# Performance work log

Hardware: AMD Instinct MI355X
Metric: run time of the kernel (lower is better)

## Reference

```python
import jax, jax.numpy as jnp
import numpy as np
import math

H = 1024
B = 16
DEPTH = 5
BEAM = 3
EPS = 1e-5  # nn.LayerNorm default eps
UCB_C = 1.414


def setup_inputs() -> dict:
    key = jax.random.key(0)
    ks = jax.random.split(key, 8)
    return {
        "problem_embedding": jax.random.normal(ks[0], (B, H), jnp.float32),
        "context": jax.random.normal(ks[1], (B, H), jnp.float32),
        # thought_encoder: Linear(2H -> H) + GELU + LayerNorm(H)
        "W_te": jax.random.normal(ks[2], (2 * H, H), jnp.float32) / math.sqrt(2 * H),
        "b_te": jnp.zeros((H,), jnp.float32),
        "g_ln": jnp.ones((H,), jnp.float32),
        "b_ln": jnp.zeros((H,), jnp.float32),
        # value_head: Linear(H -> 1)
        "w_v": jax.random.normal(ks[3], (H,), jnp.float32) / math.sqrt(H),
        "b_v": jnp.zeros((), jnp.float32),
        # expansion_net: beam_width x [Linear(H->2H), GELU, Linear(2H->H)], stacked
        "W1": jax.random.normal(ks[4], (BEAM, 2 * H, H), jnp.float32) / math.sqrt(H),
        "b1": jnp.zeros((BEAM, 2 * H), jnp.float32),
        "W2": jax.random.normal(ks[5], (BEAM, H, 2 * H), jnp.float32) / math.sqrt(2 * H),
        "b2": jnp.zeros((BEAM, H), jnp.float32),
        "num_simulations": 25,
    }


def _gelu(x):
    return jax.nn.gelu(x, approximate=False)  # torch nn.GELU default = exact erf


def _layernorm(x, g, b):
    mu = jnp.mean(x, -1, keepdims=True)
    var = jnp.mean((x - mu) ** 2, -1, keepdims=True)
    return g * (x - mu) * jax.lax.rsqrt(var + EPS) + b


def _forward(problem_embedding, context, W_te, b_te, g_ln, b_ln, w_v, b_v, W1, b1, W2, b2, num_simulations):
    MAX = 1 + num_simulations * DEPTH * BEAM  # upper bound on tree size
    BP = int(math.ceil(math.log(MAX) / math.log(BEAM))) + 2  # parent-chain length bound
    neg_inf = jnp.float32(-jnp.inf)

    def value(e):
        return e @ w_v + b_v

    def search(p, c):
        root = _layernorm(_gelu(jnp.concatenate([p, c]) @ W_te + b_te), g_ln, b_ln)
        emb = jnp.zeros((MAX, H), jnp.float32).at[0].set(root)
        vals = jnp.zeros((MAX,), jnp.float32).at[0].set(value(root))
        visits = jnp.zeros((MAX,), jnp.int32).at[0].set(1)
        n = jnp.int32(1)

        def sim(carry, _):
            emb, vals, visits, n = carry
            cur = jnp.int32(0)
            for d in range(DEPTH):
                cur_emb = emb[cur]
                # expansion condition exactly as in torch (len(tree)-1 < (idx+1)*beam)
                expand = (n - 1) < (cur + 1) * BEAM
                h = _gelu(jnp.einsum('whd,d->wh', W1, cur_emb) + b1)      # [BEAM, 2H]
                new_emb = cur_emb + 0.1 * (jnp.einsum('wdh,wh->wd', W2, h) + b2)  # [BEAM, H]
                new_vals = new_emb @ w_v + b_v                             # [BEAM]
                idx = jnp.where(expand, n + jnp.arange(BEAM, dtype=jnp.int32), MAX)
                emb = emb.at[idx].set(new_emb, mode='drop')
                vals = vals.at[idx].set(new_vals, mode='drop')
                visits = visits.at[idx].set(1, mode='drop')
                n = n + jnp.where(expand, BEAM, 0).astype(jnp.int32)
                if d < DEPTH - 1:
                    # parent_visits = sum(visits[cur*beam : (cur+1)*beam]) (python slice clamps to len)
                    pidx = cur * BEAM + jnp.arange(BEAM, dtype=jnp.int32)
                    pv = jnp.sum(jnp.where(pidx < n, visits[jnp.minimum(pidx, MAX - 1)], 0))
                    log_pv = jnp.log(jnp.maximum(pv, 1).astype(jnp.float32))
                    best_idx, best = cur, neg_inf
                    for ci in range(BEAM):
                        child = cur * BEAM + 1 + ci
                        safe = jnp.minimum(child, MAX - 1)
                        cn = jnp.maximum(visits[safe], 1).astype(jnp.float32)  # visits >= 1 always
                        ucb = vals[safe] + UCB_C * jnp.sqrt(log_pv / cn)
                        ucb = jnp.where(child < n, ucb, neg_inf)
                        better = ucb > best
                        best = jnp.where(better, ucb, best)
                        best_idx = jnp.where(better, child, best_idx)
                    cur = best_idx
            leaf = jnp.minimum(cur, n - 1)
            leaf_val = vals[leaf]

            def bp(_, st):
                node, vals_, visits_ = st
                parent = (node - 1) // BEAM
                active = node > 0
                pc = visits_[parent].astype(jnp.float32)
                upd = (vals_[parent] * pc + leaf_val) / (pc + 1.0)
                vals_ = jnp.where(active, vals_.at[parent].set(upd), vals_)
                visits_ = jnp.where(active, visits_.at[parent].add(1), visits_)
                node = jnp.where(active, parent, node)
                return node, vals_, visits_

            _, vals, visits = jax.lax.fori_loop(0, BP, bp, (leaf, vals, visits))
            visits = visits.at[leaf].add(1)
            return (emb, vals, visits, n), None

        (emb, vals, visits, n), _ = jax.lax.scan(sim, (emb, vals, visits, n), None, length=num_simulations)
        mvals = jnp.where(jnp.arange(MAX) < n, vals, neg_inf)
        best = jnp.argmax(mvals)  # first max, matching strict-> loop
        return emb[best], mvals[best]

    final_emb, best_vals = jax.vmap(search)(problem_embedding, context)
    confidence = jnp.minimum(best_vals / (jnp.max(best_vals) + 1e-8), 1.0)[:, None]
    return final_emb, confidence, best_vals


def reference(problem_embedding, context, W_te, b_te, g_ln, b_ln, w_v, b_v, W1, b1, W2, b2, num_simulations):
    return _forward(problem_embedding, context, W_te, b_te, g_ln, b_ln, w_v, b_v,
                    W1, b1, W2, b2, int(num_simulations))
```

## Files before the change

kernel.cpp:

```cpp
#include <hip/hip_runtime.h>
#include <hip/hip_fp16.h>

#define Hh 1024
#define H2 2048
#define NB 16
#define MAXN 376
#define NSTAGE 125

__device__ __forceinline__ float gelu_f(float x) {
    return 0.5f * x * (1.0f + erff(x * 0.70710678118654752440f));
}

__global__ __launch_bounds__(256) void kcvt(const float* __restrict__ src,
                                            __half* __restrict__ dst, int n) {
    int i = blockIdx.x * 256 + threadIdx.x;
    int stride = gridDim.x * 256;
    for (; i < n; i += stride) dst[i] = __float2half(src[i]);
}

__global__ __launch_bounds__(256) void k0a(const float* __restrict__ Wte,
                                           const float* __restrict__ bte,
                                           const float* __restrict__ pe,
                                           const float* __restrict__ cte,
                                           float* __restrict__ tmp) {
    __shared__ float red[8][8][33];
    int tid = threadIdx.x;
    int ob = blockIdx.x & 31, bg = blockIdx.x >> 5;
    int o_l = tid & 31, kc = tid >> 5;
    int o = ob * 32 + o_l;
    float acc[8] = {0.f,0.f,0.f,0.f,0.f,0.f,0.f,0.f};
    const float* src = (kc < 4) ? pe : cte;
    int koff = (kc < 4) ? 0 : 1024;
    int k0 = kc * 256;
    for (int k = k0; k < k0 + 256; k += 4) {
        float w0 = Wte[(size_t)(k + 0) * Hh + o];
        float w1 = Wte[(size_t)(k + 1) * Hh + o];
        float w2 = Wte[(size_t)(k + 2) * Hh + o];
        float w3 = Wte[(size_t)(k + 3) * Hh + o];
#pragma unroll
        for (int bb = 0; bb < 8; ++bb) {
            int b = bg * 8 + bb;
            const float4 x4 = *(const float4*)(src + (size_t)b * Hh + (k - koff));
            acc[bb] = fmaf(w3, x4.w, fmaf(w2, x4.z, fmaf(w1, x4.y, fmaf(w0, x4.x, acc[bb]))));
        }
    }
#pragma unroll
    for (int bb = 0; bb < 8; ++bb) red[kc][bb][o_l] = acc[bb];
    __syncthreads();
    int o2 = tid & 31, bb2 = tid >> 5;
    float s = 0.f;
#pragma unroll
    for (int q = 0; q < 8; ++q) s += red[q][bb2][o2];
    int og = ob * 32 + o2;
    int b = bg * 8 + bb2;
    tmp[(size_t)b * Hh + og] = gelu_f(s + bte[og]);
}

__global__ __launch_bounds__(256) void k0b(const float* __restrict__ tmp,
                                           const float* __restrict__ g,
                                           const float* __restrict__ bl,
                                           const float* __restrict__ wv,
                                           const float* __restrict__ bv,
                                           float* __restrict__ emb,
                                           float* __restrict__ vals,
                                           int* __restrict__ visits,
                                           int* __restrict__ nbuf,
                                           int* __restrict__ curbuf,
                                           float* __restrict__ vacc) {
    __shared__ float red[256];
    int b = blockIdx.x, tid = threadIdx.x;
    for (int q = tid; q < MAXN; q += 256) {
        if (q > 0) { vals[b * MAXN + q] = 0.f; visits[b * MAXN + q] = 0; }
    }
    if (b == 0 && tid < 96) vacc[tid] = 0.f;
    float4 v = *(const float4*)(tmp + (size_t)b * Hh + tid * 4);
    red[tid] = (v.x + v.y) + (v.z + v.w);
    __syncthreads();
    for (int st = 128; st > 0; st >>= 1) { if (tid < st) red[tid] += red[tid + st]; __syncthreads(); }
    float mu = red[0] * (1.0f / 1024.0f);
    __syncthreads();
    float dx0 = v.x - mu, dx1 = v.y - mu, dx2 = v.z - mu, dx3 = v.w - mu;
    red[tid] = (dx0 * dx0 + dx1 * dx1) + (dx2 * dx2 + dx3 * dx3);
    __syncthreads();
    for (int st = 128; st > 0; st >>= 1) { if (tid < st) red[tid] += red[tid + st]; __syncthreads(); }
    float var = red[0] * (1.0f / 1024.0f);
    __syncthreads();
    float rs = rsqrtf(var + 1e-5f);
    int d0 = tid * 4;
    float r0 = g[d0 + 0] * (dx0 * rs) + bl[d0 + 0];
    float r1 = g[d0 + 1] * (dx1 * rs) + bl[d0 + 1];
    float r2 = g[d0 + 2] * (dx2 * rs) + bl[d0 + 2];
    float r3 = g[d0 + 3] * (dx3 * rs) + bl[d0 + 3];
    float4 ro; ro.x = r0; ro.y = r1; ro.z = r2; ro.w = r3;
    *(float4*)(emb + (size_t)b * MAXN * Hh + d0) = ro;
    red[tid] = (r0 * wv[d0] + r1 * wv[d0 + 1]) + (r2 * wv[d0 + 2] + r3 * wv[d0 + 3]);
    __syncthreads();
    for (int st = 128; st > 0; st >>= 1) { if (tid < st) red[tid] += red[tid + st]; __syncthreads(); }
    if (tid == 0) {
        vals[b * MAXN] = red[0] + bv[0];
        visits[b * MAXN] = 1;
        nbuf[b] = 1;
        curbuf[b] = 0;
    }
}

__global__ __launch_bounds__(256) void k_mv1(const __half* __restrict__ W1h,
                                             const float* __restrict__ b1,
                                             const float* __restrict__ emb,
                                             float* __restrict__ hbuf,
                                             const float* __restrict__ vacc_in,
                                             float* __restrict__ vacc_out,
                                             float* vals, int* visits,
                                             const int* __restrict__ nin,
                                             const int* __restrict__ curin,
                                             int* __restrict__ nout,
                                             int* __restrict__ curout,
                                             const float* __restrict__ bv, int t) {
    __shared__ float red[64][4][17];
    __shared__ int curL[NB];
    __shared__ int exS;
    int tid = threadIdx.x;
    int d = t % 5;
    if (blockIdx.x == 0 && tid < 48) vacc_out[tid] = 0.f;
    int row = tid >> 6, kpos = tid & 63;
    int o = blockIdx.x * 4 + row;
    const __half* wp = W1h + (size_t)o * Hh;
    uint4 wl0 = *(const uint4*)(wp + kpos * 8);
    uint4 wl1 = *(const uint4*)(wp + 512 + kpos * 8);
    if (tid == 0) exS = 0;
    __syncthreads();
    if (tid < NB) {
        int b = tid;
        int n_old = nin[b], cur_old = curin[b];
        int n_new = n_old;
        bool ep = false;
        float vnew0 = 0.f, vnew1 = 0.f, vnew2 = 0.f;
        if (t > 0) {
            ep = (n_old - 1) < (cur_old + 1) * 3;
            if (ep) {
                vnew0 = bv[0] + vacc_in[b * 3 + 0];
                vnew1 = bv[0] + vacc_in[b * 3 + 1];
                vnew2 = bv[0] + vacc_in[b * 3 + 2];
                n_new += 3;
            }
        }
        int cur_new = 0;
        const float* vb = vals + b * MAXN;
        const int* tb = visits + b * MAXN;
        if (d != 0) {
            int pv = 0;
#pragma unroll
            for (int i = 0; i < 3; ++i) {
                int pidx = 3 * cur_old + i;
                if (pidx < n_new) {
                    int safe = min(pidx, MAXN - 1);
                    int jj = safe - n_old;
                    int vis = (ep && jj >= 0 && jj < 3) ? 1 : tb[safe];
                    pv += vis;
                }
            }
            float log_pv = logf((float)(pv > 1 ? pv : 1));
            float best = -INFINITY; int best_idx = cur_old;
#pragma unroll
            for (int ci = 0; ci < 3; ++ci) {
                int child = 3 * cur_old + 1 + ci;
                int safe = min(child, MAXN - 1);
                int jj = safe - n_old;
                float v; int cn;
                if (ep && jj >= 0 && jj < 3) {
                    v = (jj == 0) ? vnew0 : ((jj == 1) ? vnew1 : vnew2);
                    cn = 1;
                } else { v = vb[safe]; cn = tb[safe]; }
                float cnf = (float)(cn > 1 ? cn : 1);
                float ucb = v + 1.414f * sqrtf(log_pv / cnf);
                if (child < n_new && ucb > best) { best = ucb; best_idx = child; }
            }
            cur_new = best_idx;
        } else if (t > 0 && blockIdx.x == 0) {
            float* vbw = vals + b * MAXN;
            int* tbw = visits + b * MAXN;
            int leaf = min(cur_old, n_new - 1);
            float lv = vbw[leaf];
            int node = leaf;
#pragma unroll
            for (int it = 0; it < 8; ++it) {
                if (node > 0) {
                    int p = (node - 1) / 3;
                    int pc = tbw[p];
                    float pcf = (float)pc;
                    vbw[p] = (vbw[p] * pcf + lv) / (pcf + 1.0f);
                    tbw[p] = pc + 1;
                    node = p;
                }
            }
            tbw[leaf] += 1;
        }
        bool ex = (n_new - 1) < (cur_new + 1) * 3;
        curL[b] = cur_new;
        if (ex) atomicOr(&exS, 1 << b);
        if (blockIdx.x == 0) {
            nout[b] = n_new; curout[b] = cur_new;
            if (ep) {
                if (n_old + 0 < MAXN) { vals[b * MAXN + n_old + 0] = vnew0; visits[b * MAXN + n_old + 0] = 1; }
                if (n_old + 1 < MAXN) { vals[b * MAXN + n_old + 1] = vnew1; visits[b * MAXN + n_old + 1] = 1; }
                if (n_old + 2 < MAXN) { vals[b * MAXN + n_old + 2] = vnew2; visits[b * MAXN + n_old + 2] = 1; }
            }
        }
    }
    __syncthreads();
    unsigned em = (unsigned)exS;
    float acc[16];
#pragma unroll
    for (int b = 0; b < 16; ++b) acc[b] = 0.f;
    if (em) {
        const float4* xp[16];
#pragma unroll
        for (int b = 0; b < 16; ++b)
            xp[b] = (const float4*)(emb + (size_t)(b * MAXN + curL[b]) * Hh);
        union { uint4 u; __half h[8]; } wu[2];
        wu[0].u = wl0; wu[1].u = wl1;
#pragma unroll
        for (int j = 0; j < 2; ++j) {
            float wf[8];
#pragma unroll
            for (int r = 0; r < 8; ++r) wf[r] = __half2float(wu[j].h[r]);
            int f4 = j * 128 + kpos * 2;
#pragma unroll
            for (int b = 0; b < 16; ++b) {
                if (em & (1u << b)) {
                    float4 xa = xp[b][f4];
                    float4 xb = xp[b][f4 + 1];
                    acc[b] = fmaf(wf[3], xa.w, fmaf(wf[2], xa.z, fmaf(wf[1], xa.y, fmaf(wf[0], xa.x, acc[b]))));
                    acc[b] = fmaf(wf[7], xb.w, fmaf(wf[6], xb.z, fmaf(wf[5], xb.y, fmaf(wf[4], xb.x, acc[b]))));
                }
            }
        }
    }
    {
        float* rp = red[kpos][row];
#pragma unroll
        for (int b = 0; b < 16; ++b) rp[b] = acc[b];
    }
    __syncthreads();
    if (tid < 64) {
        int row2 = tid >> 4, b2 = tid & 15;
        if (em & (1u << b2)) {
            float s = 0.f;
#pragma unroll
            for (int q = 0; q < 64; ++q) s += red[q][row2][b2];
            int og = blockIdx.x * 4 + row2;
            int w = og >> 11, ii = og & 2047;
            float hv = gelu_f(s + b1[og]);
            hbuf[(size_t)(b2 * 3 + w) * H2 + ii] = hv;
        }
    }
}

__global__ __launch_bounds__(256) void k_mv2(const __half* __restrict__ W2h,
                                             const float* __restrict__ b2p,
                                             const float* __restrict__ wv,
                                             const float* __restrict__ hbuf,
                                             float* __restrict__ emb,
                                             float* __restrict__ vacc,
                                             const int* __restrict__ nin,
                                             const int* __restrict__ curin) {
    __shared__ float red[128][2][17];
    __shared__ float prS[16][3];
    __shared__ int curL[NB], nL[NB];
    __shared__ int exS;
    int tid = threadIdx.x;
    int row = tid >> 7, kpos = tid & 127;
    int o = blockIdx.x * 2 + row;
    const __half* wp = W2h + (size_t)o * H2;
    uint4 wl0 = *(const uint4*)(wp + kpos * 8);
    uint4 wl1 = *(const uint4*)(wp + 1024 + kpos * 8);
    if (tid < NB) { curL[tid] = curin[tid]; nL[tid] = nin[tid]; }
    __syncthreads();
    if (tid == 0) {
        int m = 0;
        for (int b = 0; b < NB; ++b)
            if ((nL[b] - 1) < (curL[b] + 1) * 3) m |= 1 << b;
        exS = m;
    }
    __syncthreads();
    unsigned em = (unsigned)exS;
    int w = o >> 10;
    float acc[16];
#pragma unroll
    for (int b = 0; b < 16; ++b) acc[b] = 0.f;
    if (em) {
        const float4* hp[16];
#pragma unroll
        for (int b = 0; b < 16; ++b) hp[b] = (const float4*)(hbuf + (size_t)(b * 3 + w) * H2);
        union { uint4 u; __half h[8]; } wu[2];
        wu[0].u = wl0; wu[1].u = wl1;
#pragma unroll
        for (int j = 0; j < 2; ++j) {
            float wf[8];
#pragma unroll
            for (int r = 0; r < 8; ++r) wf[r] = __half2float(wu[j].h[r]);
            int f4 = j * 256 + kpos * 2;
#pragma unroll
            for (int b = 0; b < 16; ++b) {
                if (em & (1u << b)) {
                    float4 ha = hp[b][f4];
                    float4 hb = hp[b][f4 + 1];
                    acc[b] = fmaf(wf[3], ha.w, fmaf(wf[2], ha.z, fmaf(wf[1], ha.y, fmaf(wf[0], ha.x, acc[b]))));
                    acc[b] = fmaf(wf[7], hb.w, fmaf(wf[6], hb.z, fmaf(wf[5], hb.y, fmaf(wf[4], hb.x, acc[b]))));
                }
            }
        }
    }
    {
        float* rp = red[kpos][row];
#pragma unroll
        for (int b = 0; b < 16; ++b) rp[b] = acc[b];
    }
    __syncthreads();
    if (tid < 32) {
        int row2 = tid >> 4, b2 = tid & 15;
        int og = blockIdx.x * 2 + row2;
        int w2i = og >> 10, d2 = og & 1023;
        float pr = 0.f;
        if (em & (1u << b2)) {
            float s = 0.f;
#pragma unroll
            for (int q = 0; q < 128; ++q) s += red[q][row2][b2];
            float ce = emb[(size_t)(b2 * MAXN + curL[b2]) * Hh + d2];
            float nv = ce + 0.1f * (s + b2p[og]);
            int nidx = nL[b2] + w2i;
            if (nidx < MAXN) emb[(size_t)(b2 * MAXN + nidx) * Hh + d2] = nv;
            pr = nv * wv[d2];
        }
        prS[b2][row2] = pr;
    }
    __syncthreads();
    if (tid < NB) {
        if (em & (1u << tid)) {
            float s = prS[tid][0] + prS[tid][1];
            int wblk = (blockIdx.x * 2) >> 10;
            atomicAdd(&vacc[tid * 3 + wblk], s);
        }
    }
}

__global__ __launch_bounds__(256) void kf(const float* __restrict__ emb,
                                          float* vals, int* visits,
                                          const int* __restrict__ nin,
                                          const int* __restrict__ curin,
                                          const float* __restrict__ vacc,
                                          const float* __restrict__ bv,
                                          float* __restrict__ out) {
    __shared__ int nF[NB];
    __shared__ float bval[NB];
    __shared__ int bidx[NB];
    __shared__ float redv[NB][16];
    __shared__ int redi[NB][16];
    __shared__ float mxS;
    int tid = threadIdx.x;
    if (tid < NB) {
        int b = tid;
        int n_old = nin[b], cur_old = curin[b];
        int n_new = n_old;
        bool ep = (n_old - 1) < (cur_old + 1) * 3;
        if (ep) {
            float vn0 = bv[0] + vacc[b * 3 + 0];
            float vn1 = bv[0] + vacc[b * 3 + 1];
            float vn2 = bv[0] + vacc[b * 3 + 2];
            if (n_old + 0 < MAXN) { vals[b * MAXN + n_old + 0] = vn0; visits[b * MAXN + n_old + 0] = 1; }
            if (n_old + 1 < MAXN) { vals[b * MAXN + n_old + 1] = vn1; visits[b * MAXN + n_old + 1] = 1; }
            if (n_old + 2 < MAXN) { vals[b * MAXN + n_old + 2] = vn2; visits[b * MAXN + n_old + 2] = 1; }
            n_new += 3;
        }
        int leaf = min(cur_old, n_new - 1);
        float lv = vals[b * MAXN + leaf];
        int node = leaf;
#pragma unroll
        for (int it = 0; it < 8; ++it) {
            if (node > 0) {
                int p = (node - 1) / 3;
                int pc = visits[b * MAXN + p];
                float pcf = (float)pc;
                vals[b * MAXN + p] = (vals[b * MAXN + p] * pcf + lv) / (pcf + 1.0f);
                visits[b * MAXN + p] = pc + 1;
                node = p;
            }
        }
        visits[b * MAXN + leaf] += 1;
        nF[b] = n_new;
    }
    __syncthreads();
    {
        int b = tid >> 4, q = tid & 15;
        float bv_ = -INFINITY; int bi_ = MAXN;
        int nn = nF[b];
        for (int idx = q; idx < MAXN; idx += 16) {
            float v = (idx < nn) ? vals[b * MAXN + idx] : -INFINITY;
            if (v > bv_ || (v == bv_ && idx < bi_)) { bv_ = v; bi_ = idx; }
        }
        redv[b][q] = bv_; redi[b][q] = bi_;
    }
    __syncthreads();
    if (tid < NB) {
        int b = tid;
        float bb = -INFINITY; int bi = MAXN;
        for (int q = 0; q < 16; ++q) {
            float v = redv[b][q]; int i2 = redi[b][q];
            if (v > bb || (v == bb && i2 < bi)) { bb = v; bi = i2; }
        }
        bval[b] = bb; bidx[b] = bi;
    }
    __syncthreads();
    if (tid == 0) {
        float m = bval[0];
        for (int b = 1; b < NB; ++b) m = fmaxf(m, bval[b]);
        mxS = m;
    }
    __syncthreads();
    if (tid < NB) {
        float c = bval[tid] / (mxS + 1e-8f);
        out[16384 + tid] = fminf(c, 1.0f);
        out[16400 + tid] = bval[tid];
    }
    for (int q2 = tid; q2 < 16384; q2 += 256) {
        int b = q2 >> 10, dd = q2 & 1023;
        out[q2] = emb[(size_t)(b * MAXN + bidx[b]) * Hh + dd];
    }
}

extern "C" void kernel_launch(void* const* d_in, const int* in_sizes, int n_in,
                              void* d_out, int out_size, void* d_ws, size_t ws_size,
                              hipStream_t stream) {
    const float* pe  = (const float*)d_in[0];
    const float* ce  = (const float*)d_in[1];
    const float* Wte = (const float*)d_in[2];
    const float* bte = (const float*)d_in[3];
    const float* gln = (const float*)d_in[4];
    const float* bln = (const float*)d_in[5];
    const float* wv  = (const float*)d_in[6];
    const float* bv  = (const float*)d_in[7];
    const float* W1  = (const float*)d_in[8];
    const float* b1  = (const float*)d_in[9];
    const float* W2  = (const float*)d_in[10];
    const float* b2  = (const float*)d_in[11];
    float* out = (float*)d_out;

    float* ws = (float*)d_ws;
    __half* W1h = (__half*)ws;
    __half* W2h = W1h + 6291456;
    float* embb = ws + 6291456;
    float* hbuf = embb + 6160384;
    float* vacc = hbuf + 98304;
    float* tmp  = vacc + 96;
    float* vals = tmp + 16384;
    int* visits = (int*)(vals + 6016);
    int* nbuf   = visits + 6016;
    int* curbuf = nbuf + 32;

    hipLaunchKernelGGL(kcvt, dim3(2048), dim3(256), 0, stream, W1, W1h, 6291456);
    hipLaunchKernelGGL(kcvt, dim3(2048), dim3(256), 0, stream, W2, W2h, 6291456);

    hipLaunchKernelGGL(k0a, dim3(64), dim3(256), 0, stream, Wte, bte, pe, ce, tmp);
    hipLaunchKernelGGL(k0b, dim3(16), dim3(256), 0, stream, tmp, gln, bln, wv, bv,
                       embb, vals, visits, nbuf, curbuf, vacc);

    for (int t = 0; t < NSTAGE; ++t) {
        int si = t & 1, so = si ^ 1;
        bool dead = (t > 0) && (t % 5 == 0);
        hipLaunchKernelGGL(k_mv1, dim3(dead ? 1 : 1536), dim3(256), 0, stream,
                           W1h, b1, embb, hbuf,
                           vacc + ((t ^ 1) & 1) * 48,
                           vacc + (t & 1) * 48,
                           vals, visits,
                           nbuf + si * 16, curbuf + si * 16,
                           nbuf + so * 16, curbuf + so * 16, bv, t);
        if (!dead)
            hipLaunchKernelGGL(k_mv2, dim3(1536), dim3(256), 0, stream,
                               W2h, b2, wv, hbuf, embb,
                               vacc + (t & 1) * 48,
                               nbuf + so * 16, curbuf + so * 16);
    }
    hipLaunchKernelGGL(kf, dim3(1), dim3(256), 0, stream,
                       embb, vals, visits, nbuf + 16, curbuf + 16, vacc, bv, out);
}
```

Baseline: 3.409 ms.

## Fold dead backprop stage into adjacent matvec kernels and prewarm fp16 weights

Removes the single-block dead launch at each simulation boundary. Its backpropagation is now recomputed locally in k_mv1, with root-level stats held in registers, and committed to global memory by block 0 of the following k_mv2. This needs triple-buffered n/cur state. A warm-up kernel also reads both fp16 weight copies to prime the cache before the loop. The cost is added control-flow complexity and a redundant read pass over the weights.

```diff
diff --git a/kernel.cpp b/kernel.cpp
--- a/kernel.cpp
+++ b/kernel.cpp
@@ -16,6 +16,16 @@
     int i = blockIdx.x * 256 + threadIdx.x;
     int stride = gridDim.x * 256;
     for (; i < n; i += stride) dst[i] = __float2half(src[i]);
+}
+
+__global__ __launch_bounds__(256) void kwarm(const uint4* __restrict__ a,
+                                             const uint4* __restrict__ b,
+                                             int n16, float* __restrict__ sink) {
+    int i = blockIdx.x * 256 + threadIdx.x;
+    int s = gridDim.x * 256;
+    unsigned acc = 0;
+    for (int j = i; j < n16; j += s) { uint4 x = a[j]; uint4 y = b[j]; acc ^= x.x ^ y.x; }
+    if (acc == 0xdeadbeefu) sink[0] = 1.f;
 }
 
 __global__ __launch_bounds__(256) void k0a(const float* __restrict__ Wte,
@@ -108,20 +118,20 @@
                                              const float* __restrict__ b1,
                                              const float* __restrict__ emb,
                                              float* __restrict__ hbuf,
-                                             const float* __restrict__ vacc_in,
-                                             float* __restrict__ vacc_out,
+                                             const float* __restrict__ vin,
+                                             float* __restrict__ vout,
                                              float* vals, int* visits,
                                              const int* __restrict__ nin,
                                              const int* __restrict__ curin,
                                              int* __restrict__ nout,
                                              int* __restrict__ curout,
-                                             const float* __restrict__ bv, int t) {
+                                             const float* __restrict__ bv, int t, int fold) {
     __shared__ float red[64][4][17];
     __shared__ int curL[NB];
     __shared__ int exS;
     int tid = threadIdx.x;
     int d = t % 5;
-    if (blockIdx.x == 0 && tid < 48) vacc_out[tid] = 0.f;
+    if (blockIdx.x == 0 && tid < 48) vout[tid] = 0.f;
     int row = tid >> 6, kpos = tid & 63;
     int o = blockIdx.x * 4 + row;
     const __half* wp = W1h + (size_t)o * Hh;
@@ -132,15 +142,45 @@
     if (tid < NB) {
         int b = tid;
         int n_old = nin[b], cur_old = curin[b];
+        float val03[4]; int vis03[4];
+        bool lcl = false;
+        if (fold) {
+            bool epA = (n_old - 1) < (cur_old + 1) * 3;
+            float a0 = 0.f, a1 = 0.f, a2 = 0.f;
+            if (epA) { a0 = bv[0] + vin[b*3+0]; a1 = bv[0] + vin[b*3+1]; a2 = bv[0] + vin[b*3+2]; }
+            int nA = n_old + (epA ? 3 : 0);
+#pragma unroll
+            for (int i = 0; i < 4; ++i) { val03[i] = vals[b*MAXN+i]; vis03[i] = visits[b*MAXN+i]; }
+            int leaf = min(cur_old, nA - 1);
+            int jl = leaf - n_old;
+            float lv;
+            if (epA && jl >= 0 && jl < 3) lv = (jl == 0) ? a0 : ((jl == 1) ? a1 : a2);
+            else lv = vals[b*MAXN + min(leaf, MAXN-1)];
+            int node = leaf;
+#pragma unroll
+            for (int it2 = 0; it2 < 8; ++it2) {
+                if (node > 0) {
+                    int p = (node - 1) / 3;
+                    int pc; float pvv;
+                    if (p < 4) { pc = vis03[p]; pvv = val03[p]; }
+                    else { pc = visits[b*MAXN+p]; pvv = vals[b*MAXN+p]; }
+                    float pcf = (float)pc;
+                    float nvv = (pvv * pcf + lv) / (pcf + 1.0f);
+                    if (p < 4) { val03[p] = nvv; vis03[p] = pc + 1; }
+                    node = p;
+                }
+            }
+            n_old = nA; cur_old = 0; lcl = true;
+        }
         int n_new = n_old;
         bool ep = false;
         float vnew0 = 0.f, vnew1 = 0.f, vnew2 = 0.f;
-        if (t > 0) {
+        if (t > 0 && !fold) {
             ep = (n_old - 1) < (cur_old + 1) * 3;
             if (ep) {
-                vnew0 = bv[0] + vacc_in[b * 3 + 0];
-                vnew1 = bv[0] + vacc_in[b * 3 + 1];
-                vnew2 = bv[0] + vacc_in[b * 3 + 2];
+                vnew0 = bv[0] + vin[b*3+0];
+                vnew1 = bv[0] + vin[b*3+1];
+                vnew2 = bv[0] + vin[b*3+2];
                 n_new += 3;
             }
         }
@@ -155,7 +195,10 @@
                 if (pidx < n_new) {
                     int safe = min(pidx, MAXN - 1);
                     int jj = safe - n_old;
-                    int vis = (ep && jj >= 0 && jj < 3) ? 1 : tb[safe];
+                    int vis;
+                    if (ep && jj >= 0 && jj < 3) vis = 1;
+                    else if (lcl && safe < 4) vis = vis03[safe];
+                    else vis = tb[safe];
                     pv += vis;
                 }
             }
@@ -170,30 +213,14 @@
                 if (ep && jj >= 0 && jj < 3) {
                     v = (jj == 0) ? vnew0 : ((jj == 1) ? vnew1 : vnew2);
                     cn = 1;
+                } else if (lcl && safe < 4) {
+                    v = val03[safe]; cn = vis03[safe];
                 } else { v = vb[safe]; cn = tb[safe]; }
                 float cnf = (float)(cn > 1 ? cn : 1);
                 float ucb = v + 1.414f * sqrtf(log_pv / cnf);
                 if (child < n_new && ucb > best) { best = ucb; best_idx = child; }
             }
             cur_new = best_idx;
-        } else if (t > 0 && blockIdx.x == 0) {
-            float* vbw = vals + b * MAXN;
-            int* tbw = visits + b * MAXN;
-            int leaf = min(cur_old, n_new - 1);
-            float lv = vbw[leaf];
-            int node = leaf;
-#pragma unroll
-            for (int it = 0; it < 8; ++it) {
-                if (node > 0) {
-                    int p = (node - 1) / 3;
-                    int pc = tbw[p];
-                    float pcf = (float)pc;
-                    vbw[p] = (vbw[p] * pcf + lv) / (pcf + 1.0f);
-                    tbw[p] = pc + 1;
-                    node = p;
-                }
-            }
-            tbw[leaf] += 1;
         }
         bool ex = (n_new - 1) < (cur_new + 1) * 3;
         curL[b] = cur_new;
@@ -263,12 +290,47 @@
                                              float* __restrict__ emb,
                                              float* __restrict__ vacc,
                                              const int* __restrict__ nin,
-                                             const int* __restrict__ curin) {
+                                             const int* __restrict__ curin,
+                                             int foldA,
+                                             const int* __restrict__ ninA,
+                                             const int* __restrict__ curinA,
+                                             const float* __restrict__ vinA,
+                                             float* vals, int* visits,
+                                             const float* __restrict__ bv) {
     __shared__ float red[128][2][17];
     __shared__ float prS[16][3];
     __shared__ int curL[NB], nL[NB];
     __shared__ int exS;
     int tid = threadIdx.x;
+    if (foldA && blockIdx.x == 0 && tid < NB) {
+        int b = tid;
+        int nO = ninA[b], cO = curinA[b];
+        bool epA = (nO - 1) < (cO + 1) * 3;
+        if (epA) {
+            float a0 = bv[0] + vinA[b*3+0];
+            float a1 = bv[0] + vinA[b*3+1];
+            float a2 = bv[0] + vinA[b*3+2];
+            if (nO + 0 < MAXN) { vals[b*MAXN+nO+0] = a0; visits[b*MAXN+nO+0] = 1; }
+            if (nO + 1 < MAXN) { vals[b*MAXN+nO+1] = a1; visits[b*MAXN+nO+1] = 1; }
+            if (nO + 2 < MAXN) { vals[b*MAXN+nO+2] = a2; visits[b*MAXN+nO+2] = 1; }
+        }
+        int nA = nO + (epA ? 3 : 0);
+        int leaf = min(cO, nA - 1);
+        float lv = vals[b*MAXN + min(leaf, MAXN-1)];
+        int node = leaf;
+#pragma unroll
+        for (int it2 = 0; it2 < 8; ++it2) {
+            if (node > 0) {
+                int p = (node - 1) / 3;
+                int pc = visits[b*MAXN+p];
+                float pcf = (float)pc;
+                vals[b*MAXN+p] = (vals[b*MAXN+p] * pcf + lv) / (pcf + 1.0f);
+                visits[b*MAXN+p] = pc + 1;
+                node = p;
+            }
+        }
+        visits[b*MAXN+leaf] += 1;
+    }
     int row = tid >> 7, kpos = tid & 127;
     int o = blockIdx.x * 2 + row;
     const __half* wp = W2h + (size_t)o * H2;
@@ -455,31 +517,40 @@
     float* vals = tmp + 16384;
     int* visits = (int*)(vals + 6016);
     int* nbuf   = visits + 6016;
-    int* curbuf = nbuf + 32;
+    int* curbuf = nbuf + 48;
+    float* sink = (float*)(curbuf + 48);
 
     hipLaunchKernelGGL(kcvt, dim3(2048), dim3(256), 0, stream, W1, W1h, 6291456);
     hipLaunchKernelGGL(kcvt, dim3(2048), dim3(256), 0, stream, W2, W2h, 6291456);
+    hipLaunchKernelGGL(kwarm, dim3(2048), dim3(256), 0, stream,
+                       (const uint4*)W1h, (const uint4*)W2h, 786432, sink);
 
     hipLaunchKernelGGL(k0a, dim3(64), dim3(256), 0, stream, Wte, bte, pe, ce, tmp);
     hipLaunchKernelGGL(k0b, dim3(16), dim3(256), 0, stream, tmp, gln, bln, wv, bv,
                        embb, vals, visits, nbuf, curbuf, vacc);
 
+    int L = 0;
     for (int t = 0; t < NSTAGE; ++t) {
-        int si = t & 1, so = si ^ 1;
-        bool dead = (t > 0) && (t % 5 == 0);
-        hipLaunchKernelGGL(k_mv1, dim3(dead ? 1 : 1536), dim3(256), 0, stream,
+        if (t > 0 && t % 5 == 0) continue;
+        int fold = (t % 5 == 1 && t > 1) ? 1 : 0;
+        int rs = (fold ? (t - 1) : t) % 3;
+        int wsS = (t + 1) % 3;
+        int vi = ((L + 1) & 1) * 48;
+        int vo = (L & 1) * 48;
+        hipLaunchKernelGGL(k_mv1, dim3(1536), dim3(256), 0, stream,
                            W1h, b1, embb, hbuf,
-                           vacc + ((t ^ 1) & 1) * 48,
-                           vacc + (t & 1) * 48,
+                           vacc + vi, vacc + vo,
                            vals, visits,
-                           nbuf + si * 16, curbuf + si * 16,
-                           nbuf + so * 16, curbuf + so * 16, bv, t);
-        if (!dead)
-            hipLaunchKernelGGL(k_mv2, dim3(1536), dim3(256), 0, stream,
-                               W2h, b2, wv, hbuf, embb,
-                               vacc + (t & 1) * 48,
-                               nbuf + so * 16, curbuf + so * 16);
+                           nbuf + rs * 16, curbuf + rs * 16,
+                           nbuf + wsS * 16, curbuf + wsS * 16, bv, t, fold);
+        hipLaunchKernelGGL(k_mv2, dim3(1536), dim3(256), 0, stream,
+                           W2h, b2, wv, hbuf, embb,
+                           vacc + vo,
+                           nbuf + wsS * 16, curbuf + wsS * 16,
+                           fold, nbuf + rs * 16, curbuf + rs * 16, vacc + vi,
+                           vals, visits, bv);
+        ++L;
     }
     hipLaunchKernelGGL(kf, dim3(1), dim3(256), 0, stream,
-                       embb, vals, visits, nbuf + 16, curbuf + 16, vacc, bv, out);
-}
+                       embb, vals, visits, nbuf + 32, curbuf + 32, vacc, bv, out);
+}
```

New measurement: 3.412 ms. Within noise of the previous version (+0.1%).

## Split tree bookkeeping into single-block kernel and double matvec rows per block

Applied to the files above, without the earlier changes.

Moves the per-stage MCTS selection, expansion and backprop bookkeeping out of the first matvec kernel into a tiny one-block kernel. That kernel publishes a control buffer (expansion mask, current node and node count), which both matvec kernels read instead of recomputing it. The dead depth-0 stage launches are folded into the next stage's bookkeeping. Each matvec block now handles twice as many output rows with 4 weight vectors per thread, so half as many blocks are launched. This adds one small serial launch per stage in exchange for removing redundant per-block bookkeeping and skipped launches, and it lowers parallelism per launch.

```diff
diff --git a/kernel.cpp b/kernel.cpp
--- a/kernel.cpp
+++ b/kernel.cpp
@@ -72,7 +72,7 @@
     for (int q = tid; q < MAXN; q += 256) {
         if (q > 0) { vals[b * MAXN + q] = 0.f; visits[b * MAXN + q] = 0; }
     }
-    if (b == 0 && tid < 96) vacc[tid] = 0.f;
+    if (b == 0 && tid < 48) vacc[tid] = 0.f;
     float4 v = *(const float4*)(tmp + (size_t)b * Hh + tid * 4);
     red[tid] = (v.x + v.y) + (v.z + v.w);
     __syncthreads();
@@ -104,127 +104,117 @@
     }
 }
 
+__global__ __launch_bounds__(64) void kbook(float* vals, int* visits,
+                                            int* nbuf, int* curbuf,
+                                            float* vacc, int* ctrl,
+                                            const float* __restrict__ bv,
+                                            int t, int fold) {
+    __shared__ int exArr[NB];
+    int tid = threadIdx.x;
+    if (tid < NB) {
+        int b = tid;
+        int n = nbuf[b], cur = curbuf[b];
+        float* vb = vals + b * MAXN;
+        int* tb = visits + b * MAXN;
+        float v0 = vacc[b * 3 + 0], v1 = vacc[b * 3 + 1], v2 = vacc[b * 3 + 2];
+        if (fold) {
+            bool epA = (n - 1) < (cur + 1) * 3;
+            if (epA) {
+                if (n + 0 < MAXN) { vb[n + 0] = bv[0] + v0; tb[n + 0] = 1; }
+                if (n + 1 < MAXN) { vb[n + 1] = bv[0] + v1; tb[n + 1] = 1; }
+                if (n + 2 < MAXN) { vb[n + 2] = bv[0] + v2; tb[n + 2] = 1; }
+                n += 3;
+            }
+            int leaf = min(cur, n - 1);
+            float lv = vb[min(leaf, MAXN - 1)];
+            int node = leaf;
+#pragma unroll
+            for (int it = 0; it < 8; ++it) {
+                if (node > 0) {
+                    int p = (node - 1) / 3;
+                    int pc = tb[p];
+                    float pcf = (float)pc;
+                    vb[p] = (vb[p] * pcf + lv) / (pcf + 1.0f);
+                    tb[p] = pc + 1;
+                    node = p;
+                }
+            }
+            tb[leaf] += 1;
+            cur = 0;
+        } else if (t > 0) {
+            bool ep = (n - 1) < (cur + 1) * 3;
+            if (ep) {
+                if (n + 0 < MAXN) { vb[n + 0] = bv[0] + v0; tb[n + 0] = 1; }
+                if (n + 1 < MAXN) { vb[n + 1] = bv[0] + v1; tb[n + 1] = 1; }
+                if (n + 2 < MAXN) { vb[n + 2] = bv[0] + v2; tb[n + 2] = 1; }
+                n += 3;
+            }
+        }
+        int d = t % 5;
+        int cur_new = 0;
+        if (d != 0) {
+            int pv = 0;
+#pragma unroll
+            for (int i = 0; i < 3; ++i) {
+                int pidx = 3 * cur + i;
+                if (pidx < n) pv += tb[min(pidx, MAXN - 1)];
+            }
+            float log_pv = logf((float)(pv > 1 ? pv : 1));
+            float best = -INFINITY; int best_idx = cur;
+#pragma unroll
+            for (int ci = 0; ci < 3; ++ci) {
+                int child = 3 * cur + 1 + ci;
+                int safe = min(child, MAXN - 1);
+                float v = vb[safe]; int cn = tb[safe];
+                float cnf = (float)(cn > 1 ? cn : 1);
+                float ucb = v + 1.414f * sqrtf(log_pv / cnf);
+                if (child < n && ucb > best) { best = ucb; best_idx = child; }
+            }
+            cur_new = best_idx;
+        }
+        nbuf[b] = n; curbuf[b] = cur_new;
+        ctrl[1 + b] = cur_new;
+        ctrl[17 + b] = n;
+        exArr[b] = ((n - 1) < (cur_new + 1) * 3) ? 1 : 0;
+    }
+    __syncthreads();
+    if (tid == 0) {
+        int m = 0;
+        for (int b = 0; b < NB; ++b) if (exArr[b]) m |= (1 << b);
+        ctrl[0] = m;
+    }
+    if (tid < 48) vacc[tid] = 0.f;
+}
+
 __global__ __launch_bounds__(256) void k_mv1(const __half* __restrict__ W1h,
                                              const float* __restrict__ b1,
                                              const float* __restrict__ emb,
                                              float* __restrict__ hbuf,
-                                             const float* __restrict__ vacc_in,
-                                             float* __restrict__ vacc_out,
-                                             float* vals, int* visits,
-                                             const int* __restrict__ nin,
-                                             const int* __restrict__ curin,
-                                             int* __restrict__ nout,
-                                             int* __restrict__ curout,
-                                             const float* __restrict__ bv, int t) {
-    __shared__ float red[64][4][17];
-    __shared__ int curL[NB];
-    __shared__ int exS;
+                                             const int* __restrict__ ctrl) {
+    __shared__ float red[32][8][17];
     int tid = threadIdx.x;
-    int d = t % 5;
-    if (blockIdx.x == 0 && tid < 48) vacc_out[tid] = 0.f;
-    int row = tid >> 6, kpos = tid & 63;
-    int o = blockIdx.x * 4 + row;
+    int row = tid >> 5, kpos = tid & 31;
+    int o = blockIdx.x * 8 + row;
     const __half* wp = W1h + (size_t)o * Hh;
-    uint4 wl0 = *(const uint4*)(wp + kpos * 8);
-    uint4 wl1 = *(const uint4*)(wp + 512 + kpos * 8);
-    if (tid == 0) exS = 0;
-    __syncthreads();
-    if (tid < NB) {
-        int b = tid;
-        int n_old = nin[b], cur_old = curin[b];
-        int n_new = n_old;
-        bool ep = false;
-        float vnew0 = 0.f, vnew1 = 0.f, vnew2 = 0.f;
-        if (t > 0) {
-            ep = (n_old - 1) < (cur_old + 1) * 3;
-            if (ep) {
-                vnew0 = bv[0] + vacc_in[b * 3 + 0];
-                vnew1 = bv[0] + vacc_in[b * 3 + 1];
-                vnew2 = bv[0] + vacc_in[b * 3 + 2];
-                n_new += 3;
-            }
-        }
-        int cur_new = 0;
-        const float* vb = vals + b * MAXN;
-        const int* tb = visits + b * MAXN;
-        if (d != 0) {
-            int pv = 0;
-#pragma unroll
-            for (int i = 0; i < 3; ++i) {
-                int pidx = 3 * cur_old + i;
-                if (pidx < n_new) {
-                    int safe = min(pidx, MAXN - 1);
-                    int jj = safe - n_old;
-                    int vis = (ep && jj >= 0 && jj < 3) ? 1 : tb[safe];
-                    pv += vis;
-                }
-            }
-            float log_pv = logf((float)(pv > 1 ? pv : 1));
-            float best = -INFINITY; int best_idx = cur_old;
-#pragma unroll
-            for (int ci = 0; ci < 3; ++ci) {
-                int child = 3 * cur_old + 1 + ci;
-                int safe = min(child, MAXN - 1);
-                int jj = safe - n_old;
-                float v; int cn;
-                if (ep && jj >= 0 && jj < 3) {
-                    v = (jj == 0) ? vnew0 : ((jj == 1) ? vnew1 : vnew2);
-                    cn = 1;
-                } else { v = vb[safe]; cn = tb[safe]; }
-                float cnf = (float)(cn > 1 ? cn : 1);
-                float ucb = v + 1.414f * sqrtf(log_pv / cnf);
-                if (child < n_new && ucb > best) { best = ucb; best_idx = child; }
-            }
-            cur_new = best_idx;
-        } else if (t > 0 && blockIdx.x == 0) {
-            float* vbw = vals + b * MAXN;
-            int* tbw = visits + b * MAXN;
-            int leaf = min(cur_old, n_new - 1);
-            float lv = vbw[leaf];
-            int node = leaf;
-#pragma unroll
-            for (int it = 0; it < 8; ++it) {
-                if (node > 0) {
-                    int p = (node - 1) / 3;
-                    int pc = tbw[p];
-                    float pcf = (float)pc;
-                    vbw[p] = (vbw[p] * pcf + lv) / (pcf + 1.0f);
-                    tbw[p] = pc + 1;
-                    node = p;
-                }
-            }
-            tbw[leaf] += 1;
-        }
-        bool ex = (n_new - 1) < (cur_new + 1) * 3;
-        curL[b] = cur_new;
-        if (ex) atomicOr(&exS, 1 << b);
-        if (blockIdx.x == 0) {
-            nout[b] = n_new; curout[b] = cur_new;
-            if (ep) {
-                if (n_old + 0 < MAXN) { vals[b * MAXN + n_old + 0] = vnew0; visits[b * MAXN + n_old + 0] = 1; }
-                if (n_old + 1 < MAXN) { vals[b * MAXN + n_old + 1] = vnew1; visits[b * MAXN + n_old + 1] = 1; }
-                if (n_old + 2 < MAXN) { vals[b * MAXN + n_old + 2] = vnew2; visits[b * MAXN + n_old + 2] = 1; }
-            }
-        }
-    }
-    __syncthreads();
-    unsigned em = (unsigned)exS;
-    float acc[16];
-#pragma unroll
-    for (int b = 0; b < 16; ++b) acc[b] = 0.f;
+    uint4 wl[4];
+#pragma unroll
+    for (int j = 0; j < 4; ++j) wl[j] = *(const uint4*)(wp + j * 256 + kpos * 8);
+    unsigned em = (unsigned)ctrl[0];
     if (em) {
         const float4* xp[16];
 #pragma unroll
         for (int b = 0; b < 16; ++b)
-            xp[b] = (const float4*)(emb + (size_t)(b * MAXN + curL[b]) * Hh);
-        union { uint4 u; __half h[8]; } wu[2];
-        wu[0].u = wl0; wu[1].u = wl1;
-#pragma unroll
-        for (int j = 0; j < 2; ++j) {
+            xp[b] = (const float4*)(emb + (size_t)(b * MAXN + ctrl[1 + b]) * Hh);
+        float acc[16];
+#pragma unroll
+        for (int b = 0; b < 16; ++b) acc[b] = 0.f;
+#pragma unroll
+        for (int j = 0; j < 4; ++j) {
+            union { uint4 u; __half h[8]; } wu; wu.u = wl[j];
             float wf[8];
 #pragma unroll
-            for (int r = 0; r < 8; ++r) wf[r] = __half2float(wu[j].h[r]);
-            int f4 = j * 128 + kpos * 2;
+            for (int r = 0; r < 8; ++r) wf[r] = __half2float(wu.h[r]);
+            int f4 = j * 64 + kpos * 2;
 #pragma unroll
             for (int b = 0; b < 16; ++b) {
                 if (em & (1u << b)) {
@@ -235,20 +225,18 @@
                 }
             }
         }
-    }
-    {
         float* rp = red[kpos][row];
 #pragma unroll
         for (int b = 0; b < 16; ++b) rp[b] = acc[b];
     }
     __syncthreads();
-    if (tid < 64) {
+    if (em && tid < 128) {
         int row2 = tid >> 4, b2 = tid & 15;
         if (em & (1u << b2)) {
             float s = 0.f;
 #pragma unroll
-            for (int q = 0; q < 64; ++q) s += red[q][row2][b2];
-            int og = blockIdx.x * 4 + row2;
+            for (int q = 0; q < 32; ++q) s += red[q][row2][b2];
+            int og = blockIdx.x * 8 + row2;
             int w = og >> 11, ii = og & 2047;
             float hv = gelu_f(s + b1[og]);
             hbuf[(size_t)(b2 * 3 + w) * H2 + ii] = hv;
@@ -262,44 +250,33 @@
                                              const float* __restrict__ hbuf,
                                              float* __restrict__ emb,
                                              float* __restrict__ vacc,
-                                             const int* __restrict__ nin,
-                                             const int* __restrict__ curin) {
-    __shared__ float red[128][2][17];
-    __shared__ float prS[16][3];
-    __shared__ int curL[NB], nL[NB];
-    __shared__ int exS;
+                                             const int* __restrict__ ctrl) {
+    __shared__ float red[64][4][17];
+    __shared__ float prS[16][5];
     int tid = threadIdx.x;
-    int row = tid >> 7, kpos = tid & 127;
-    int o = blockIdx.x * 2 + row;
+    int row = tid >> 6, kpos = tid & 63;
+    int o = blockIdx.x * 4 + row;
     const __half* wp = W2h + (size_t)o * H2;
-    uint4 wl0 = *(const uint4*)(wp + kpos * 8);
-    uint4 wl1 = *(const uint4*)(wp + 1024 + kpos * 8);
-    if (tid < NB) { curL[tid] = curin[tid]; nL[tid] = nin[tid]; }
-    __syncthreads();
-    if (tid == 0) {
-        int m = 0;
-        for (int b = 0; b < NB; ++b)
-            if ((nL[b] - 1) < (curL[b] + 1) * 3) m |= 1 << b;
-        exS = m;
-    }
-    __syncthreads();
-    unsigned em = (unsigned)exS;
+    uint4 wl[4];
+#pragma unroll
+    for (int j = 0; j < 4; ++j) wl[j] = *(const uint4*)(wp + j * 512 + kpos * 8);
+    unsigned em = (unsigned)ctrl[0];
     int w = o >> 10;
-    float acc[16];
-#pragma unroll
-    for (int b = 0; b < 16; ++b) acc[b] = 0.f;
     if (em) {
         const float4* hp[16];
 #pragma unroll
-        for (int b = 0; b < 16; ++b) hp[b] = (const float4*)(hbuf + (size_t)(b * 3 + w) * H2);
-        union { uint4 u; __half h[8]; } wu[2];
-        wu[0].u = wl0; wu[1].u = wl1;
-#pragma unroll
-        for (int j = 0; j < 2; ++j) {
+        for (int b = 0; b < 16; ++b)
+            hp[b] = (const float4*)(hbuf + (size_t)(b * 3 + w) * H2);
+        float acc[16];
+#pragma unroll
+        for (int b = 0; b < 16; ++b) acc[b] = 0.f;
+#pragma unroll
+        for (int j = 0; j < 4; ++j) {
+            union { uint4 u; __half h[8]; } wu; wu.u = wl[j];
             float wf[8];
 #pragma unroll
-            for (int r = 0; r < 8; ++r) wf[r] = __half2float(wu[j].h[r]);
-            int f4 = j * 256 + kpos * 2;
+            for (int r = 0; r < 8; ++r) wf[r] = __half2float(wu.h[r]);
+            int f4 = j * 128 + kpos * 2;
 #pragma unroll
             for (int b = 0; b < 16; ++b) {
                 if (em & (1u << b)) {
@@ -310,37 +287,32 @@
                 }
             }
         }
-    }
-    {
         float* rp = red[kpos][row];
 #pragma unroll
         for (int b = 0; b < 16; ++b) rp[b] = acc[b];
     }
     __syncthreads();
-    if (tid < 32) {
+    if (em && tid < 64) {
         int row2 = tid >> 4, b2 = tid & 15;
-        int og = blockIdx.x * 2 + row2;
+        int og = blockIdx.x * 4 + row2;
         int w2i = og >> 10, d2 = og & 1023;
         float pr = 0.f;
         if (em & (1u << b2)) {
             float s = 0.f;
 #pragma unroll
-            for (int q = 0; q < 128; ++q) s += red[q][row2][b2];
-            float ce = emb[(size_t)(b2 * MAXN + curL[b2]) * Hh + d2];
+            for (int q = 0; q < 64; ++q) s += red[q][row2][b2];
+            float ce = emb[(size_t)(b2 * MAXN + ctrl[1 + b2]) * Hh + d2];
             float nv = ce + 0.1f * (s + b2p[og]);
-            int nidx = nL[b2] + w2i;
+            int nidx = ctrl[17 + b2] + w2i;
             if (nidx < MAXN) emb[(size_t)(b2 * MAXN + nidx) * Hh + d2] = nv;
             pr = nv * wv[d2];
         }
         prS[b2][row2] = pr;
     }
     __syncthreads();
-    if (tid < NB) {
-        if (em & (1u << tid)) {
-            float s = prS[tid][0] + prS[tid][1];
-            int wblk = (blockIdx.x * 2) >> 10;
-            atomicAdd(&vacc[tid * 3 + wblk], s);
-        }
+    if (em && tid < NB && (em & (1u << tid))) {
+        float s = prS[tid][0] + prS[tid][1] + prS[tid][2] + prS[tid][3];
+        atomicAdd(&vacc[tid * 3 + w], s);
     }
 }
 
@@ -451,11 +423,12 @@
     float* embb = ws + 6291456;
     float* hbuf = embb + 6160384;
     float* vacc = hbuf + 98304;
-    float* tmp  = vacc + 96;
+    float* tmp  = vacc + 48;
     float* vals = tmp + 16384;
     int* visits = (int*)(vals + 6016);
     int* nbuf   = visits + 6016;
-    int* curbuf = nbuf + 32;
+    int* curbuf = nbuf + 16;
+    int* ctrl   = curbuf + 16;
 
     hipLaunchKernelGGL(kcvt, dim3(2048), dim3(256), 0, stream, W1, W1h, 6291456);
     hipLaunchKernelGGL(kcvt, dim3(2048), dim3(256), 0, stream, W2, W2h, 6291456);
@@ -465,21 +438,15 @@
                        embb, vals, visits, nbuf, curbuf, vacc);
 
     for (int t = 0; t < NSTAGE; ++t) {
-        int si = t & 1, so = si ^ 1;
-        bool dead = (t > 0) && (t % 5 == 0);
-        hipLaunchKernelGGL(k_mv1, dim3(dead ? 1 : 1536), dim3(256), 0, stream,
-                           W1h, b1, embb, hbuf,
-                           vacc + ((t ^ 1) & 1) * 48,
-                           vacc + (t & 1) * 48,
-                           vals, visits,
-                           nbuf + si * 16, curbuf + si * 16,
-                           nbuf + so * 16, curbuf + so * 16, bv, t);
-        if (!dead)
-            hipLaunchKernelGGL(k_mv2, dim3(1536), dim3(256), 0, stream,
-                               W2h, b2, wv, hbuf, embb,
-                               vacc + (t & 1) * 48,
-                               nbuf + so * 16, curbuf + so * 16);
+        if (t > 0 && t % 5 == 0) continue;
+        int fold = (t % 5 == 1 && t > 1) ? 1 : 0;
+        hipLaunchKernelGGL(kbook, dim3(1), dim3(64), 0, stream,
+                           vals, visits, nbuf, curbuf, vacc, ctrl, bv, t, fold);
+        hipLaunchKernelGGL(k_mv1, dim3(768), dim3(256), 0, stream,
+                           W1h, b1, embb, hbuf, ctrl);
+        hipLaunchKernelGGL(k_mv2, dim3(768), dim3(256), 0, stream,
+                           W2h, b2, wv, hbuf, embb, vacc, ctrl);
     }
     hipLaunchKernelGGL(kf, dim3(1), dim3(256), 0, stream,
-                       embb, vals, visits, nbuf + 16, curbuf + 16, vacc, bv, out);
-}
+                       embb, vals, visits, nbuf, curbuf, vacc, bv, out);
+}
```

Measured after the change: 3.113 ms. 1.09x faster.
